# Optimization experiments

Hardware: AMD Instinct MI355X
Metric: run time of the kernel (lower is better)

## Reference

```python
import jax, jax.numpy as jnp
import numpy as np

B, SY, SX, CIN = 16, 180, 360, 16
WIDTH, MODES = 32, 32


def _vandermonde(pos, modes):
    # Nonuniform DFT matrix V[k, n] = exp(-2*pi*i * k * p_n) / sqrt(L),
    # positions normalized to [0, 1). Inverse uses conj(V) (near-unitary).
    p = (pos - pos.min()) / (pos.max() - pos.min())
    k = jnp.arange(modes, dtype=jnp.float32)
    V = jnp.exp(-2j * jnp.pi * k[:, None] * p[None, :]) / jnp.sqrt(jnp.float32(pos.shape[0]))
    return V.astype(jnp.complex64)


def _spectral(h, fw1, fw2, Vy, Vx):
    # h: [B, C, M, N]; Vy: [modes, M]; Vx: [modes, N]
    hc = h.astype(jnp.complex64)
    w1 = fw1[..., 0] + 1j * fw1[..., 1]  # [I, O, modes] complex
    w2 = fw2[..., 0] + 1j * fw2[..., 1]
    # y-direction: forward transform over M, mix channels per mode, inverse
    fty = jnp.einsum('bimn,km->bink', hc, Vy)          # [B, I, N, modes]
    oy = jnp.einsum('bink,iok->bonk', fty, w1)          # [B, O, N, modes]
    xy = jnp.einsum('bonk,km->bomn', oy, jnp.conj(Vy)).real
    # x-direction: forward transform over N
    ftx = jnp.einsum('bimn,kn->bimk', hc, Vx)           # [B, I, M, modes]
    ox = jnp.einsum('bimk,iok->bomk', ftx, w2)          # [B, O, M, modes]
    xx = jnp.einsum('bomk,kn->bomn', ox, jnp.conj(Vx)).real
    return xx + xy


def gelu(v):
    return jax.nn.gelu(v, approximate=False)  # torch F.gelu default (erf)


def setup_inputs() -> dict:
    key = jax.random.key(0)
    ks = jax.random.split(key, 16)
    s = 1.0 / (WIDTH * WIDTH)
    return {
        'x': jax.random.normal(ks[0], (B, SY, SX, CIN), jnp.float32),
        'sparse_x': jnp.sort(jax.random.uniform(ks[1], (SX,), jnp.float32)),
        'sparse_y': jnp.sort(jax.random.uniform(ks[2], (SY,), jnp.float32)),
        'fc0_w': jax.random.normal(ks[3], (CIN + 2, WIDTH), jnp.float32) * 0.1,
        'fc0_b': jnp.zeros((WIDTH,), jnp.float32),
        'fw1': jax.random.uniform(ks[4], (4, WIDTH, WIDTH, MODES, 2), jnp.float32) * s,
        'fw2': jax.random.uniform(ks[5], (4, WIDTH, WIDTH, MODES, 2), jnp.float32) * s,
        'w1': jax.random.normal(ks[6], (4, WIDTH, WIDTH), jnp.float32) * 0.1,
        'b1': jnp.zeros((4, WIDTH), jnp.float32),
        'w2': jax.random.normal(ks[7], (4, WIDTH, WIDTH), jnp.float32) * 0.1,
        'b2': jnp.zeros((4, WIDTH), jnp.float32),
        'fc1_w': jax.random.normal(ks[8], (WIDTH, 128), jnp.float32) * 0.1,
        'fc1_b': jnp.zeros((128,), jnp.float32),
        'fc2_w': jax.random.normal(ks[9], (128, 1), jnp.float32) * 0.1,
        'fc2_b': jnp.zeros((1,), jnp.float32),
    }


def reference(x, sparse_x, sparse_y, fc0_w, fc0_b, fw1, fw2, w1, b1, w2, b2,
              fc1_w, fc1_b, fc2_w, fc2_b):
    b, sy, sx, _ = x.shape
    # get_grid (faithful to source: (p - min)/max)
    gx = (sparse_x - sparse_x.min()) / sparse_x.max()          # [SX]
    gy = (sparse_y - sparse_y.min()) / sparse_y.max()          # [SY]
    grid = jnp.stack([jnp.broadcast_to(gx[None, :], (sy, sx)),
                      jnp.broadcast_to(gy[:, None], (sy, sx))], axis=-1)
    grid = jnp.broadcast_to(grid[None], (b, sy, sx, 2))
    h = jnp.concatenate([x, grid], axis=-1) @ fc0_w + fc0_b    # [B, SY, SX, W]
    h = jnp.transpose(h, (0, 3, 1, 2))                         # [B, W, SY, SX]

    Vy = _vandermonde(sparse_y, MODES)
    Vx = _vandermonde(sparse_x, MODES)

    for i in range(4):
        x1 = _spectral(h, fw1[i], fw2[i], Vy, Vx)
        x2 = jnp.einsum('bcmn,oc->bomn', x1, w1[i]) + b1[i][None, :, None, None]
        x4 = jnp.einsum('bcmn,oc->bomn', gelu(x2), w2[i]) + b2[i][None, :, None, None]
        h = (gelu(x4) if i < 3 else x4) + h  # last block: no gelu on x4 (per source)

    h = jnp.transpose(h, (0, 2, 3, 1))                         # [B, SY, SX, W]
    h = gelu(h @ fc1_w + fc1_b)
    return h @ fc2_w + fc2_b                                   # [B, SY, SX, 1]
```

## Files before the change

### kernel.cpp

```cpp
#include <hip/hip_runtime.h>
#include <math.h>

#define NB 16
#define NSY 180
#define NSX 360
#define NCIN 16
#define NW 32
#define NMODES 32
#define NPIX (NSY*NSX)
#define NPTS (NB*NPIX)

typedef unsigned int uint;
typedef unsigned short ushort;
typedef __attribute__((ext_vector_type(8))) short bf16x8;
typedef __attribute__((ext_vector_type(4))) float f32x4;

union U4 { uint u[4]; bf16x8 v; };

__device__ __forceinline__ float gelu_f(float v){
  float u = v*(-2.3021681f - 0.10295335f*v*v);
  return v * __builtin_amdgcn_rcpf(1.f + exp2f(u));
}
__device__ __forceinline__ ushort f2bf(float x){
  uint u = __float_as_uint(x);
  return (ushort)((u + 0x7FFFu + ((u>>16)&1u)) >> 16);
}
__device__ __forceinline__ uint packbf2(float a, float b){
  uint r;
  asm("v_cvt_pk_bf16_f32 %0, %1, %2" : "=v"(r) : "v"(a), "v"(b));
  return r;
}
__device__ __forceinline__ float bf2f(ushort u){
  return __uint_as_float(((uint)u) << 16);
}
__device__ __forceinline__ uint addbf2(uint h, uint a){
  return packbf2(bf2f((ushort)(h & 0xffffu)) + bf2f((ushort)(a & 0xffffu)),
                 bf2f((ushort)(h >> 16))     + bf2f((ushort)(a >> 16)));
}

__global__ __launch_bounds__(256) void k_setup(const float* __restrict__ sx,
    const float* __restrict__ sy, const float* __restrict__ fc1_w,
    const float* __restrict__ w2m, const float* __restrict__ fw1,
    const float* __restrict__ fw2, const float* __restrict__ w1m,
    const float* __restrict__ x, const float* __restrict__ fc0_w,
    const float* __restrict__ fc0_b,
    ushort* __restrict__ Abfy, ushort* __restrict__ Abfx,
    ushort* __restrict__ VyCT, ushort* __restrict__ VxCT,
    ushort* __restrict__ f1Tbf, ushort* __restrict__ w2bf,
    ushort* __restrict__ wAbf, ushort* __restrict__ hbf){
  int bid = blockIdx.x;
  if (bid < 96){
    int idx = bid*256 + threadIdx.x;
    float sx0 = sx[0], sxL = sx[NSX-1];
    float sy0 = sy[0], syL = sy[NSY-1];
    const float scy = 0.07453559924999298980f;
    const float scx = 0.05270462766947298886f;
    if (idx < 64*192){
      int kri = idx/192, m = idx%192;
      float val = 0.f;
      if (m < NSY){
        int k = kri>>1;
        float p = (sy[m]-sy0)/(syL-sy0);
        float ang = -6.2831853071795864769f*(float)k*p;
        val = ((kri&1)? sinf(ang) : cosf(ang))*scy;
      }
      Abfy[idx] = f2bf(val);
    }
    if (idx < 192*64){
      int m = idx/64, kri = idx%64;
      float val = 0.f;
      if (m < NSY){
        int k = kri>>1;
        float p = (sy[m]-sy0)/(syL-sy0);
        float ang = -6.2831853071795864769f*(float)k*p;
        val = ((kri&1)? sinf(ang) : cosf(ang))*scy;
      }
      VyCT[idx] = f2bf(val);
    }
    if (idx < 64*384){
      int kri = idx/384, n = idx%384;
      float val = 0.f;
      if (n < NSX){
        int k = kri>>1;
        float p = (sx[n]-sx0)/(sxL-sx0);
        float ang = -6.2831853071795864769f*(float)k*p;
        val = ((kri&1)? sinf(ang) : cosf(ang))*scx;
      }
      Abfx[idx] = f2bf(val);
    }
    if (idx < 384*64){
      int n = idx/64, kri = idx%64;
      float val = 0.f;
      if (n < NSX){
        int k = kri>>1;
        float p = (sx[n]-sx0)/(sxL-sx0);
        float ang = -6.2831853071795864769f*(float)k*p;
        val = ((kri&1)? sinf(ang) : cosf(ang))*scx;
      }
      VxCT[idx] = f2bf(val);
    }
    if (idx < 128*32){
      int j = idx >> 5, c = idx & 31;
      f1Tbf[idx] = f2bf(fc1_w[c*128 + j]);
    }
    if (idx < 4096){
      w2bf[idx] = f2bf(w2m[idx]);
    }
  } else if (bid < 96 + 1024){
    int id = (bid-96)*256 + threadIdx.x;
    int half = id >> 17;
    int r = id & 131071;
    int i  = r >> 15;
    int in = (r >> 10) & 31;
    int k  = (r >> 5) & 31;
    int o  = r & 31;
    const float* src = half ? fw2 : fw1;
    const float* wm  = w1m + i*1024 + o*32;
    const float* sp  = src + ((size_t)((i*32+in)*1024 + k))*2;
    float sR = 0.f, sI = 0.f;
    #pragma unroll
    for (int c=0;c<32;c++){
      float w = wm[c];
      sR += w * sp[c*64];
      sI += w * sp[c*64+1];
    }
    ushort rH = f2bf(sR);  ushort rL = f2bf(sR - bf2f(rH));
    ushort iH = f2bf(sI);  ushort iL = f2bf(sI - bf2f(iH));
    ushort nH = f2bf(-sI); ushort nL = f2bf(-sI - bf2f(nH));
    ushort* base = wAbf + (((size_t)((i*2 + half)*32 + k)) << 13);
    int oi = o*64 + 2*in;
    base[oi]          = rH;  base[oi+1]        = nH;
    base[2048 + oi]   = rL;  base[2048 + oi+1] = nL;
    base[4096 + oi]   = iH;  base[4096 + oi+1] = rH;
    base[6144 + oi]   = iL;  base[6144 + oi+1] = rL;
  } else {
    int p = (bid-1120)*256 + threadIdx.x;
    if (p >= NPTS) return;
    int b = p/NPIX, r = p%NPIX, m = r/NSX, n = r%NSX;
    const float* xp = x + (size_t)p*NCIN;
    float4 x0 = *(const float4*)(xp);
    float4 x1 = *(const float4*)(xp+4);
    float4 x2 = *(const float4*)(xp+8);
    float4 x3 = *(const float4*)(xp+12);
    float xv[NCIN+2] = {x0.x,x0.y,x0.z,x0.w, x1.x,x1.y,x1.z,x1.w,
                        x2.x,x2.y,x2.z,x2.w, x3.x,x3.y,x3.z,x3.w, 0.f,0.f};
    xv[16] = (sx[n]-sx[0])/sx[NSX-1];
    xv[17] = (sy[m]-sy[0])/sy[NSY-1];
    float acc[NW];
    #pragma unroll
    for (int o=0;o<NW;o++) acc[o] = fc0_b[o];
    #pragma unroll
    for (int j=0;j<NCIN+2;j++){
      float v = xv[j];
      #pragma unroll
      for (int o=0;o<NW;o++) acc[o] += v*fc0_w[j*32+o];
    }
    ushort* hq = hbf + (size_t)b*NW*NPIX + r;
    #pragma unroll
    for (int o=0;o<NW;o++) hq[(size_t)o*NPIX] = f2bf(acc[o]);
  }
}

__global__ __launch_bounds__(256) void k_fwd(const ushort* __restrict__ hbf,
    const ushort* __restrict__ Abfy, const ushort* __restrict__ Abfx,
    uint* __restrict__ fty, uint* __restrict__ ftx, int b0, int ylim){
  __shared__ ushort rawS[2][32*64];
  __shared__ uint   BtS[2][64*18];
  int bx = blockIdx.x;
  int tid = threadIdx.x;
  int l = tid & 63, g = tid >> 6;
  int c15 = l & 15, q = l >> 4;
  if (bx < ylim){
    int nt6 = bx % 6; int c = (bx/6) & 31; int bb = bx/192;
    int n0 = nt6*64;
    const ushort* hb = hbf + (size_t)((b0+bb)*NW + c)*NPIX;
    int yr = tid >> 3, yc = (tid & 7) << 3;
    auto ldY = [&](int ks)->uint4{
      int m = ks*32 + yr;
      int gc = n0 + yc;
      uint4 p = {0u,0u,0u,0u};
      if (m < NSY && gc < NSX) p = *(const uint4*)(hb + (size_t)m*NSX + gc);
      return p;
    };
    bf16x8 afr[6];
    #pragma unroll
    for (int ks=0; ks<6; ks++)
      afr[ks] = *(const bf16x8*)(Abfy + (size_t)(16*g + c15)*192 + ks*32 + q*8);
    f32x4 acc[4];
    #pragma unroll
    for (int t=0;t<4;t++) acc[t] = (f32x4){0.f,0.f,0.f,0.f};
    uint4 pre0 = ldY(0);
    uint4 pre1 = ldY(1);
    #pragma unroll
    for (int ks=0; ks<6; ks++){
      uint4 cur = (ks&1) ? pre1 : pre0;
      *(uint4*)(&rawS[ks&1][(size_t)tid*8]) = cur;
      if (ks < 4){
        if (ks&1) pre1 = ldY(ks+2); else pre0 = ldY(ks+2);
      }
      const ushort* rp = rawS[ks&1];
      ushort v[8];
      #pragma unroll
      for (int j=0;j<8;j++) v[j] = rp[(8*g + j)*64 + l];
      #pragma unroll
      for (int i=0;i<4;i++)
        BtS[ks&1][l*18 + 4*g + i] = (uint)v[2*i] | ((uint)v[2*i+1] << 16);
      __syncthreads();
      #pragma unroll
      for (int nt=0; nt<4; nt++){
        const uint* bp = &BtS[ks&1][(nt*16 + c15)*18 + q*4];
        U4 bu;
        uint2 lo = *(const uint2*)(bp);
        uint2 hi = *(const uint2*)(bp+2);
        bu.u[0]=lo.x; bu.u[1]=lo.y; bu.u[2]=hi.x; bu.u[3]=hi.y;
        acc[nt] = __builtin_amdgcn_mfma_f32_16x16x32_bf16(afr[ks], bu.v, acc[nt], 0,0,0);
      }
    }
    uint* fb = fty + (size_t)(bb*NW + c)*32*NSX;
    int k0 = 8*g + 2*q;
    #pragma unroll
    for (int nt=0; nt<4; nt++){
      int nn = n0 + nt*16 + c15;
      if (nn < NSX){
        fb[(size_t)k0*NSX + nn]     = packbf2(acc[nt][0], acc[nt][1]);
        fb[(size_t)(k0+1)*NSX + nn] = packbf2(acc[nt][2], acc[nt][3]);
      }
    }
  } else {
    int t = bx - ylim;
    int mt = t % 3; int c = (t/3) & 31; int bb = t/96;
    int m0 = mt*64;
    const ushort* hb = hbf + (size_t)((b0+bb)*NW + c)*NPIX;
    int xr = tid >> 2, xc = (tid & 3) << 3;
    auto ldX = [&](int ks)->uint4{
      int m = m0 + xr;
      int n = ks*32 + xc;
      uint4 p = {0u,0u,0u,0u};
      if (m < NSY && n < NSX) p = *(const uint4*)(hb + (size_t)m*NSX + n);
      return p;
    };
    auto ldA = [&](int ks)->bf16x8{
      return *(const bf16x8*)(Abfx + (size_t)(16*g + c15)*384 + ks*32 + q*8);
    };
    f32x4 acc[4];
    #pragma unroll
    for (int tt=0;tt<4;tt++) acc[tt] = (f32x4){0.f,0.f,0.f,0.f};
    uint4 pre0 = ldX(0), pre1 = ldX(1);
    bf16x8 a0 = ldA(0), a1 = ldA(1);
    int s4 = (tid & 3) * 4;
    #pragma unroll
    for (int ks=0; ks<12; ks++){
      uint4 cur = (ks&1) ? pre1 : pre0;
      bf16x8 af = (ks&1) ? a1 : a0;
      uint* btp = &BtS[ks&1][xr*18 + s4];
      btp[0] = cur.x; btp[1] = cur.y; btp[2] = cur.z; btp[3] = cur.w;
      if (ks < 10){
        if (ks&1){ pre1 = ldX(ks+2); a1 = ldA(ks+2); }
        else     { pre0 = ldX(ks+2); a0 = ldA(ks+2); }
      }
      __syncthreads();
      #pragma unroll
      for (int nt=0; nt<4; nt++){
        const uint* bp = &BtS[ks&1][(nt*16 + c15)*18 + q*4];
        U4 bu;
        uint2 lo = *(const uint2*)(bp);
        uint2 hi = *(const uint2*)(bp+2);
        bu.u[0]=lo.x; bu.u[1]=lo.y; bu.u[2]=hi.x; bu.u[3]=hi.y;
        acc[nt] = __builtin_amdgcn_mfma_f32_16x16x32_bf16(af, bu.v, acc[nt], 0,0,0);
      }
    }
    uint* fb = ftx + (size_t)(bb*NW + c)*32*NSY;
    int k0 = 8*g + 2*q;
    #pragma unroll
    for (int nt=0; nt<4; nt++){
      int mm = m0 + nt*16 + c15;
      if (mm < NSY){
        fb[(size_t)k0*NSY + mm]     = packbf2(acc[nt][0], acc[nt][1]);
        fb[(size_t)(k0+1)*NSY + mm] = packbf2(acc[nt][2], acc[nt][3]);
      }
    }
  }
}

__global__ __launch_bounds__(256) void k_mix2(const uint* __restrict__ fty,
    const uint* __restrict__ ftx, const ushort* __restrict__ wA,
    uint* __restrict__ oy, uint* __restrict__ ox, int ylim){
  int bx = blockIdx.x;
  const uint* ft; uint* oo; int Nlen, NT, k, bb, halfoff;
  if (bx < ylim){
    bb = bx >> 5; k = bx & 31; ft = fty; oo = oy; Nlen = NSX; NT = 23; halfoff = 0;
  } else {
    int t = bx - ylim;
    bb = t >> 5; k = t & 31; ft = ftx; oo = ox; Nlen = NSY; NT = 12; halfoff = 262144;
  }
  int tid = threadIdx.x;
  int g = tid >> 6, l = tid & 63;
  int c15 = l & 15, q = l >> 4;
  const ushort* wk = wA + halfoff + k*8192;
  bf16x8 af[2][2][2][2];
  #pragma unroll
  for (int mt=0;mt<2;mt++)
    #pragma unroll
    for (int s=0;s<2;s++)
      #pragma unroll
      for (int ps=0;ps<2;ps++)
        #pragma unroll
        for (int pr=0;pr<2;pr++)
          af[mt][s][ps][pr] = *(const bf16x8*)(wk + ps*4096 + pr*2048
                                               + (mt*16+c15)*64 + s*32 + q*8);
  const uint* fb = ft + ((size_t)bb*1024 + (size_t)k)*Nlen;
  uint* ob = oo + ((size_t)bb*1024 + (size_t)k)*Nlen;
  auto ldB = [&](int nt, U4* bu){
    int n = nt*16 + c15; if (n >= Nlen) n = Nlen-1;
    #pragma unroll
    for (int s=0;s<2;s++)
      #pragma unroll
      for (int t=0;t<4;t++){
        int in = s*16 + q*4 + t;
        bu[s].u[t] = fb[(size_t)in*32*Nlen + n];
      }
  };
  U4 pre[2], cur[2];
  ldB(g, pre);
  for (int nt = g; nt < NT; nt += 4){
    cur[0] = pre[0]; cur[1] = pre[1];
    if (nt + 4 < NT) ldB(nt+4, pre);
    f32x4 acc[2][2];
    #pragma unroll
    for (int mt=0;mt<2;mt++)
      #pragma unroll
      for (int ps=0;ps<2;ps++)
        acc[mt][ps] = (f32x4){0.f,0.f,0.f,0.f};
    #pragma unroll
    for (int s=0;s<2;s++)
      #pragma unroll
      for (int mt=0;mt<2;mt++)
        #pragma unroll
        for (int ps=0;ps<2;ps++){
          acc[mt][ps] = __builtin_amdgcn_mfma_f32_16x16x32_bf16(af[mt][s][ps][0], cur[s].v, acc[mt][ps], 0,0,0);
          acc[mt][ps] = __builtin_amdgcn_mfma_f32_16x16x32_bf16(af[mt][s][ps][1], cur[s].v, acc[mt][ps], 0,0,0);
        }
    int n = nt*16 + c15;
    if (n < Nlen){
      #pragma unroll
      for (int mt=0;mt<2;mt++)
        #pragma unroll
        for (int r2=0;r2<4;r2++){
          int o = mt*16 + q*4 + r2;
          ob[(size_t)o*32*Nlen + n] = packbf2(acc[mt][0][r2], acc[mt][1][r2]);
        }
    }
  }
}

__global__ __launch_bounds__(256) void k_inv(const uint* __restrict__ oyb,
    const uint* __restrict__ oxb, const ushort* __restrict__ VyCT,
    const ushort* __restrict__ VxCT, const float* __restrict__ b1,
    ushort* __restrict__ x2bf){
  __shared__ uint Bt[64*34];
  int bx = blockIdx.x;
  int c8 = bx & 7; int rr = bx >> 3; int slot = rr/6; int nt6 = rr - slot*6;
  int gid = slot*8 + c8;
  int bb = gid >> 5; int o = gid & 31;
  int n0 = nt6*64;
  int tid = threadIdx.x;
  int l = tid & 63, g = tid >> 6;
  int c15 = l & 15, q = l >> 4;
  const uint* oxp = oxb + (size_t)(bb*NW + o)*32*NSY;
  const uint* oyp = oyb + (size_t)(bb*NW + o)*32*NSX;
  #pragma unroll
  for (int i=0;i<8;i++){
    int idx = tid + i*256;
    int k = idx >> 6, n = idx & 63;
    int ng = n0 + n;
    Bt[n*34 + k] = (ng < NSX) ? oyp[(size_t)k*NSX + ng] : 0u;
  }
  __syncthreads();
  f32x4 acc[3][4];
  #pragma unroll
  for (int mt=0;mt<3;mt++)
    #pragma unroll
    for (int nt=0;nt<4;nt++) acc[mt][nt] = (f32x4){0.f,0.f,0.f,0.f};
  #pragma unroll
  for (int s=0;s<4;s++){
    bf16x8 bfr[4];
    #pragma unroll
    for (int nt=0;nt<4;nt++){
      if (s < 2){
        const uint* bp = &Bt[(nt*16 + c15)*34 + s*16 + q*4];
        U4 bu; uint2 lo = *(const uint2*)bp; uint2 hi = *(const uint2*)(bp+2);
        bu.u[0]=lo.x; bu.u[1]=lo.y; bu.u[2]=hi.x; bu.u[3]=hi.y;
        bfr[nt] = bu.v;
      } else {
        bfr[nt] = *(const bf16x8*)(VxCT + (size_t)(n0 + nt*16 + c15)*64 + (s-2)*32 + q*8);
      }
    }
    #pragma unroll
    for (int mt=0;mt<3;mt++){
      int mrow = g*48 + mt*16 + c15;
      bf16x8 afr;
      if (s < 2){
        afr = *(const bf16x8*)(VyCT + (size_t)mrow*64 + s*32 + q*8);
      } else {
        int mc = mrow < NSY ? mrow : (NSY-1);
        int k0 = (s-2)*16 + q*4;
        U4 au;
        #pragma unroll
        for (int j=0;j<4;j++)
          au.u[j] = oxp[(size_t)(k0+j)*NSY + mc];
        afr = au.v;
      }
      #pragma unroll
      for (int nt=0;nt<4;nt++)
        acc[mt][nt] = __builtin_amdgcn_mfma_f32_16x16x32_bf16(afr, bfr[nt], acc[mt][nt], 0,0,0);
    }
  }
  float bias = b1[o];
  ushort* xp = x2bf + (size_t)(bb*NW + o)*NPIX;
  #pragma unroll
  for (int mt=0;mt<3;mt++){
    #pragma unroll
    for (int nt=0;nt<4;nt++){
      int n = n0 + nt*16 + c15;
      if (n < NSX){
        #pragma unroll
        for (int r2=0;r2<4;r2++){
          int m = g*48 + mt*16 + q*4 + r2;
          if (m < NSY) xp[(size_t)m*NSX + n] = f2bf(gelu_f(acc[mt][nt][r2] + bias));
        }
      }
    }
  }
}

__global__ __launch_bounds__(256) void k_pw2(const ushort* __restrict__ x2bf,
    const ushort* __restrict__ w2b, const float* __restrict__ b2,
    uint* __restrict__ hbfu, int b0, int nloc){
  const int HP = NPIX/2;
  __shared__ uint Ot[32*132];
  int blk = blockIdx.x;
  int bb = blk/254, bt = blk - bb*254;
  int pxb = bt*256;
  int tid = threadIdx.x;
  int g = tid >> 6, l = tid & 63;
  int c15 = l & 15, q = l >> 4;
  bf16x8 bfr[2];
  #pragma unroll
  for (int nt=0; nt<2; nt++)
    bfr[nt] = *(const bf16x8*)(w2b + (size_t)(nt*16 + c15)*32 + q*8);
  const ushort* xb = x2bf + ((size_t)bb*NW + q*8)*NPIX;
  f32x4 acc[4][2];
  #pragma unroll
  for (int mt=0;mt<4;mt++){
    U4 au; au.u[0]=0u; au.u[1]=0u; au.u[2]=0u; au.u[3]=0u;
    int pr = pxb + g*64 + mt*16 + c15;
    if (pr < NPIX){
      ushort v[8];
      #pragma unroll
      for (int j=0;j<8;j++) v[j] = xb[(size_t)j*NPIX + pr];
      #pragma unroll
      for (int i2=0;i2<4;i2++) au.u[i2] = (uint)v[2*i2] | ((uint)v[2*i2+1] << 16);
    }
    #pragma unroll
    for (int nt=0;nt<2;nt++){
      acc[mt][nt] = (f32x4){0.f,0.f,0.f,0.f};
      acc[mt][nt] = __builtin_amdgcn_mfma_f32_16x16x32_bf16(au.v, bfr[nt], acc[mt][nt], 0,0,0);
    }
  }
  #pragma unroll
  for (int nt=0;nt<2;nt++){
    int o = nt*16 + c15;
    float bias = b2[o];
    #pragma unroll
    for (int mt=0;mt<4;mt++){
      float v0 = gelu_f(acc[mt][nt][0] + bias);
      float v1 = gelu_f(acc[mt][nt][1] + bias);
      float v2 = gelu_f(acc[mt][nt][2] + bias);
      float v3 = gelu_f(acc[mt][nt][3] + bias);
      int px2 = g*32 + mt*8 + q*2;
      uint2 w2v; w2v.x = packbf2(v0,v1); w2v.y = packbf2(v2,v3);
      *(uint2*)(&Ot[o*132 + px2]) = w2v;
    }
  }
  __syncthreads();
  int o = tid >> 3, t8 = tid & 7;
  uint* hb = hbfu + ((size_t)((b0+bb)*NW + o))*HP + (pxb>>1) + t8*16;
  const uint* lrow = &Ot[o*132 + t8*16];
  int p2g0 = (pxb>>1) + t8*16;
  #pragma unroll
  for (int jj=0; jj<16; jj+=4){
    if (p2g0 + jj + 4 <= HP){
      uint4 hv = *(const uint4*)(hb + jj);
      uint4 av = *(const uint4*)(lrow + jj);
      uint4 r;
      r.x = addbf2(hv.x, av.x); r.y = addbf2(hv.y, av.y);
      r.z = addbf2(hv.z, av.z); r.w = addbf2(hv.w, av.w);
      *(uint4*)(hb + jj) = r;
    } else {
      #pragma unroll
      for (int t=0;t<4;t++){
        if (p2g0 + jj + t < HP){
          uint hv = hb[jj+t];
          hb[jj+t] = addbf2(hv, lrow[jj+t]);
        }
      }
    }
  }
}

#define OTS 134
__global__ __launch_bounds__(256) void k_pw2f(const ushort* __restrict__ x2bf,
    const ushort* __restrict__ w2b, const float* __restrict__ b2,
    const uint* __restrict__ hbfu,
    const ushort* __restrict__ f1Tbf, const float* __restrict__ f1b,
    const float* __restrict__ f2w, const float* __restrict__ f2b,
    float* __restrict__ out, int b0){
  const int HP = NPIX/2;
  __shared__ uint Ot[32*OTS];
  int blk = blockIdx.x;
  int bb = blk/254, bt = blk - bb*254;
  int pxb = bt*256;
  int tid = threadIdx.x;
  int g = tid >> 6, l = tid & 63;
  int c15 = l & 15, q = l >> 4;
  bf16x8 bfr[2];
  #pragma unroll
  for (int nt=0; nt<2; nt++)
    bfr[nt] = *(const bf16x8*)(w2b + (size_t)(nt*16 + c15)*32 + q*8);
  const ushort* xb = x2bf + ((size_t)bb*NW + q*8)*NPIX;
  f32x4 acc[4][2];
  #pragma unroll
  for (int mt=0;mt<4;mt++){
    U4 au; au.u[0]=0u; au.u[1]=0u; au.u[2]=0u; au.u[3]=0u;
    int pr = pxb + g*64 + mt*16 + c15;
    if (pr < NPIX){
      ushort v[8];
      #pragma unroll
      for (int j=0;j<8;j++) v[j] = xb[(size_t)j*NPIX + pr];
      #pragma unroll
      for (int i2=0;i2<4;i2++) au.u[i2] = (uint)v[2*i2] | ((uint)v[2*i2+1] << 16);
    }
    #pragma unroll
    for (int nt=0;nt<2;nt++){
      acc[mt][nt] = (f32x4){0.f,0.f,0.f,0.f};
      acc[mt][nt] = __builtin_amdgcn_mfma_f32_16x16x32_bf16(au.v, bfr[nt], acc[mt][nt], 0,0,0);
    }
  }
  #pragma unroll
  for (int nt=0;nt<2;nt++){
    int o = nt*16 + c15;
    float bias = b2[o];
    #pragma unroll
    for (int mt=0;mt<4;mt++){
      float v0 = acc[mt][nt][0] + bias;
      float v1 = acc[mt][nt][1] + bias;
      float v2 = acc[mt][nt][2] + bias;
      float v3 = acc[mt][nt][3] + bias;
      int px2 = g*32 + mt*8 + q*2;
      uint2 w2v; w2v.x = packbf2(v0,v1); w2v.y = packbf2(v2,v3);
      *(uint2*)(&Ot[o*OTS + px2]) = w2v;
    }
  }
  __syncthreads();
  {
    int o = tid >> 3, t8 = tid & 7;
    const uint* hb = hbfu + ((size_t)((b0+bb)*NW + o))*HP + (pxb>>1) + t8*16;
    uint* lrow = &Ot[o*OTS + t8*16];
    int p2g0 = (pxb>>1) + t8*16;
    #pragma unroll
    for (int jj=0; jj<16; jj+=4){
      if (p2g0 + jj + 4 <= HP){
        uint4 hv = *(const uint4*)(hb + jj);
        lrow[jj+0] = addbf2(hv.x, lrow[jj+0]);
        lrow[jj+1] = addbf2(hv.y, lrow[jj+1]);
        lrow[jj+2] = addbf2(hv.z, lrow[jj+2]);
        lrow[jj+3] = addbf2(hv.w, lrow[jj+3]);
      } else {
        #pragma unroll
        for (int t=0;t<4;t++){
          if (p2g0 + jj + t < HP)
            lrow[jj+t] = addbf2(hb[jj+t], lrow[jj+t]);
        }
      }
    }
  }
  bf16x8 b1fr[8];
  #pragma unroll
  for (int nt=0; nt<8; nt++)
    b1fr[nt] = *(const bf16x8*)(f1Tbf + (size_t)(nt*16 + c15)*32 + q*8);
  __syncthreads();
  const ushort* Ts = (const ushort*)Ot;
  float fb2 = f2b[0];
  float* ob = out + (size_t)(b0+bb)*NPIX + pxb;
  #pragma unroll
  for (int mt=0;mt<4;mt++){
    int px_in = g*64 + mt*16 + c15;
    const ushort* tp = Ts + (size_t)(q*8)*(2*OTS) + px_in;
    ushort v[8];
    #pragma unroll
    for (int j2=0;j2<8;j2++) v[j2] = tp[j2*(2*OTS)];
    U4 au;
    #pragma unroll
    for (int i2=0;i2<4;i2++) au.u[i2] = (uint)v[2*i2] | ((uint)v[2*i2+1] << 16);
    f32x4 a8[8];
    #pragma unroll
    for (int nt=0; nt<8; nt++){
      a8[nt] = (f32x4){0.f,0.f,0.f,0.f};
      a8[nt] = __builtin_amdgcn_mfma_f32_16x16x32_bf16(au.v, b1fr[nt], a8[nt], 0,0,0);
    }
    float s[4] = {0.f,0.f,0.f,0.f};
    #pragma unroll
    for (int nt=0; nt<8; nt++){
      int jj = nt*16 + c15;
      float bj = f1b[jj], wj = f2w[jj];
      #pragma unroll
      for (int r2=0;r2<4;r2++) s[r2] += gelu_f(a8[nt][r2] + bj) * wj;
    }
    #pragma unroll
    for (int msk=1; msk<16; msk<<=1){
      #pragma unroll
      for (int r2=0;r2<4;r2++) s[r2] += __shfl_xor(s[r2], msk, 64);
    }
    if (c15 == 0){
      int pl = g*64 + mt*16 + q*4;
      if (pxb + pl + 4 <= NPIX){
        float4 o4 = {s[0]+fb2, s[1]+fb2, s[2]+fb2, s[3]+fb2};
        *(float4*)(ob + pl) = o4;
      }
    }
  }
}

extern "C" void kernel_launch(void* const* d_in, const int* in_sizes, int n_in,
                              void* d_out, int out_size, void* d_ws, size_t ws_size,
                              hipStream_t stream) {
  const float* x     = (const float*)d_in[0];
  const float* sx    = (const float*)d_in[1];
  const float* sy    = (const float*)d_in[2];
  const float* fc0_w = (const float*)d_in[3];
  const float* fc0_b = (const float*)d_in[4];
  const float* fw1   = (const float*)d_in[5];
  const float* fw2   = (const float*)d_in[6];
  const float* w1m   = (const float*)d_in[7];
  const float* b1    = (const float*)d_in[8];
  const float* w2m   = (const float*)d_in[9];
  const float* b2    = (const float*)d_in[10];
  const float* fc1_w = (const float*)d_in[11];
  const float* fc1_b = (const float*)d_in[12];
  const float* fc2_w = (const float*)d_in[13];
  const float* fc2_b = (const float*)d_in[14];
  float* out = (float*)d_out;

  char* wsb = (char*)d_ws;
  size_t off = 0;
  auto alloc = [&](size_t bytes)->char*{
    char* p = wsb + off;
    off = (off + bytes + 255) & ~(size_t)255;
    return p;
  };
  ushort* hbf   = (ushort*)alloc((size_t)NB*NW*NPIX*2);
  ushort* Abfy  = (ushort*)alloc(64*192*2);
  ushort* Abfx  = (ushort*)alloc(64*384*2);
  ushort* VyCT  = (ushort*)alloc(192*64*2);
  ushort* VxCT  = (ushort*)alloc(384*64*2);
  ushort* f1Tbf = (ushort*)alloc(128*32*2);
  ushort* w2bf  = (ushort*)alloc(4096*2);
  ushort* wAbf  = (ushort*)alloc((size_t)4*2*32*4*2048*2);
  const size_t fixedB = off;

  const size_t szX2  = (size_t)NW*NPIX*2;
  const size_t szFty = (size_t)NW*32*NSX*4;
  const size_t szFtx = (size_t)NW*32*NSY*4;
  const size_t szOy  = szFty, szOx = szFtx;
  const size_t perB  = szX2 + szOy + szOx;

  int NC = 16;
  while (NC > 1 && fixedB + (size_t)NC*perB + 4096 > ws_size) NC >>= 1;
  char* pb = wsb + fixedB;
  ushort* x2bf = (ushort*)pb;
  uint*   fty  = (uint*)pb;
  uint*   ftx  = (uint*)(pb + (size_t)NC*szFty);
  uint*   oy   = (uint*)(pb + (size_t)NC*szX2);
  uint*   ox   = (uint*)((char*)oy + (size_t)NC*szOy);

  k_setup<<<96 + 1024 + 4050, 256, 0, stream>>>(sx, sy, fc1_w, w2m, fw1, fw2,
                                                w1m, x, fc0_w, fc0_b,
                                                Abfy, Abfx, VyCT, VxCT,
                                                f1Tbf, w2bf, wAbf, hbf);

  for (int i=0;i<4;i++){
    for (int b0=0; b0<NB; b0+=NC){
      k_fwd<<<NC*288, 256, 0, stream>>>(hbf, Abfy, Abfx, fty, ftx, b0, NC*192);
      k_mix2<<<NC*64, 256, 0, stream>>>(fty, ftx, wAbf + (size_t)i*524288,
                                        oy, ox, NC*32);
      k_inv<<<NC*192, 256, 0, stream>>>(oy, ox, VyCT, VxCT, b1 + i*32, x2bf);
      if (i < 3){
        k_pw2<<<NC*254, 256, 0, stream>>>((const ushort*)x2bf,
                                          w2bf + (size_t)i*1024,
                                          b2 + i*32, (uint*)hbf, b0, NC);
      } else {
        k_pw2f<<<NC*254, 256, 0, stream>>>((const ushort*)x2bf,
                                           w2bf + (size_t)i*1024,
                                           b2 + i*32, (const uint*)hbf,
                                           f1Tbf, fc1_b, fc2_w, fc2_b,
                                           out, b0);
      }
    }
  }
}
```

Before: 797.0 us.

## Transpose spectral intermediate layouts so mix and inverse kernels load contiguous vectors

The forward-transform outputs (fty, ftx) are now stored channel-innermost, so the mode-mixing kernel can fetch each MFMA B fragment with two 16-byte loads instead of eight strided scalar loads. The x-branch mix output is likewise stored mode-innermost so the inverse kernel reads its A fragment with a single vector load. The cost moves to the forward kernel's stores, which now scatter with a stride of 32 words per channel and so coalesce worse. This touches three kernels that must agree on the new layout.

After: 1.160 ms. 45.5% more time.

```diff
diff --git a/kernel.cpp b/kernel.cpp
--- a/kernel.cpp
+++ b/kernel.cpp
@@ -216,14 +216,14 @@
         acc[nt] = __builtin_amdgcn_mfma_f32_16x16x32_bf16(afr[ks], bu.v, acc[nt], 0,0,0);
       }
     }
-    uint* fb = fty + (size_t)(bb*NW + c)*32*NSX;
+    uint* fb = fty + (size_t)bb*(32*NSX*32);
     int k0 = 8*g + 2*q;
     #pragma unroll
     for (int nt=0; nt<4; nt++){
       int nn = n0 + nt*16 + c15;
       if (nn < NSX){
-        fb[(size_t)k0*NSX + nn]     = packbf2(acc[nt][0], acc[nt][1]);
-        fb[(size_t)(k0+1)*NSX + nn] = packbf2(acc[nt][2], acc[nt][3]);
+        fb[((size_t)k0*NSX + nn)*32 + c]     = packbf2(acc[nt][0], acc[nt][1]);
+        fb[((size_t)(k0+1)*NSX + nn)*32 + c] = packbf2(acc[nt][2], acc[nt][3]);
       }
     }
   } else {
@@ -269,14 +269,14 @@
         acc[nt] = __builtin_amdgcn_mfma_f32_16x16x32_bf16(af, bu.v, acc[nt], 0,0,0);
       }
     }
-    uint* fb = ftx + (size_t)(bb*NW + c)*32*NSY;
+    uint* fb = ftx + (size_t)bb*(32*NSY*32);
     int k0 = 8*g + 2*q;
     #pragma unroll
     for (int nt=0; nt<4; nt++){
       int mm = m0 + nt*16 + c15;
       if (mm < NSY){
-        fb[(size_t)k0*NSY + mm]     = packbf2(acc[nt][0], acc[nt][1]);
-        fb[(size_t)(k0+1)*NSY + mm] = packbf2(acc[nt][2], acc[nt][3]);
+        fb[((size_t)k0*NSY + mm)*32 + c]     = packbf2(acc[nt][0], acc[nt][1]);
+        fb[((size_t)(k0+1)*NSY + mm)*32 + c] = packbf2(acc[nt][2], acc[nt][3]);
       }
     }
   }
@@ -286,12 +286,12 @@
     const uint* __restrict__ ftx, const ushort* __restrict__ wA,
     uint* __restrict__ oy, uint* __restrict__ ox, int ylim){
   int bx = blockIdx.x;
-  const uint* ft; uint* oo; int Nlen, NT, k, bb, halfoff;
+  const uint* ft; int Nlen, NT, k, bb, halfoff, isY;
   if (bx < ylim){
-    bb = bx >> 5; k = bx & 31; ft = fty; oo = oy; Nlen = NSX; NT = 23; halfoff = 0;
+    bb = bx >> 5; k = bx & 31; ft = fty; Nlen = NSX; NT = 23; halfoff = 0; isY = 1;
   } else {
     int t = bx - ylim;
-    bb = t >> 5; k = t & 31; ft = ftx; oo = ox; Nlen = NSY; NT = 12; halfoff = 262144;
+    bb = t >> 5; k = t & 31; ft = ftx; Nlen = NSY; NT = 12; halfoff = 262144; isY = 0;
   }
   int tid = threadIdx.x;
   int g = tid >> 6, l = tid & 63;
@@ -308,17 +308,16 @@
         for (int pr=0;pr<2;pr++)
           af[mt][s][ps][pr] = *(const bf16x8*)(wk + ps*4096 + pr*2048
                                                + (mt*16+c15)*64 + s*32 + q*8);
-  const uint* fb = ft + ((size_t)bb*1024 + (size_t)k)*Nlen;
-  uint* ob = oo + ((size_t)bb*1024 + (size_t)k)*Nlen;
+  const uint* fbT = ft + ((size_t)bb*32 + k)*Nlen*32;
+  uint* obY = oy + ((size_t)bb*1024 + (size_t)k)*NSX;
+  uint* obX = ox + (size_t)bb*32*NSY*32;
   auto ldB = [&](int nt, U4* bu){
     int n = nt*16 + c15; if (n >= Nlen) n = Nlen-1;
-    #pragma unroll
-    for (int s=0;s<2;s++)
-      #pragma unroll
-      for (int t=0;t<4;t++){
-        int in = s*16 + q*4 + t;
-        bu[s].u[t] = fb[(size_t)in*32*Nlen + n];
-      }
+    const uint* rp = fbT + (size_t)n*32 + q*4;
+    uint4 a = *(const uint4*)(rp);
+    uint4 b = *(const uint4*)(rp + 16);
+    bu[0].u[0]=a.x; bu[0].u[1]=a.y; bu[0].u[2]=a.z; bu[0].u[3]=a.w;
+    bu[1].u[0]=b.x; bu[1].u[1]=b.y; bu[1].u[2]=b.z; bu[1].u[3]=b.w;
   };
   U4 pre[2], cur[2];
   ldB(g, pre);
@@ -342,13 +341,23 @@
         }
     int n = nt*16 + c15;
     if (n < Nlen){
-      #pragma unroll
-      for (int mt=0;mt<2;mt++)
+      if (isY){
         #pragma unroll
-        for (int r2=0;r2<4;r2++){
-          int o = mt*16 + q*4 + r2;
-          ob[(size_t)o*32*Nlen + n] = packbf2(acc[mt][0][r2], acc[mt][1][r2]);
-        }
+        for (int mt=0;mt<2;mt++)
+          #pragma unroll
+          for (int r2=0;r2<4;r2++){
+            int o = mt*16 + q*4 + r2;
+            obY[(size_t)o*32*NSX + n] = packbf2(acc[mt][0][r2], acc[mt][1][r2]);
+          }
+      } else {
+        #pragma unroll
+        for (int mt=0;mt<2;mt++)
+          #pragma unroll
+          for (int r2=0;r2<4;r2++){
+            int o = mt*16 + q*4 + r2;
+            obX[((size_t)o*NSY + n)*32 + k] = packbf2(acc[mt][0][r2], acc[mt][1][r2]);
+          }
+      }
     }
   }
 }
@@ -366,8 +375,8 @@
   int tid = threadIdx.x;
   int l = tid & 63, g = tid >> 6;
   int c15 = l & 15, q = l >> 4;
-  const uint* oxp = oxb + (size_t)(bb*NW + o)*32*NSY;
-  const uint* oyp = oyb + (size_t)(bb*NW + o)*32*NSX;
+  const uint* oxp = oxb + ((size_t)bb*NW + o)*NSY*32;
+  const uint* oyp = oyb + ((size_t)bb*NW + o)*32*NSX;
   #pragma unroll
   for (int i=0;i<8;i++){
     int idx = tid + i*256;
@@ -404,10 +413,8 @@
       } else {
         int mc = mrow < NSY ? mrow : (NSY-1);
         int k0 = (s-2)*16 + q*4;
-        U4 au;
-        #pragma unroll
-        for (int j=0;j<4;j++)
-          au.u[j] = oxp[(size_t)(k0+j)*NSY + mc];
+        uint4 t4 = *(const uint4*)(oxp + (size_t)mc*32 + k0);
+        U4 au; au.u[0]=t4.x; au.u[1]=t4.y; au.u[2]=t4.z; au.u[3]=t4.w;
         afr = au.v;
       }
       #pragma unroll
```
